# Optimization experiments

Hardware: AMD Instinct MI355X
Metric: run time of the kernel (lower is better)

The kernel has to match this reference:

```python
import jax, jax.numpy as jnp
import numpy as np

NUM_VISUAL = 16
MAX_PATCH = 1024
DIM = 1280
NUM_HEADS = 16
HEAD_DIM = DIM // NUM_HEADS  # 80


def _make_rope_cache(key):
    # cos/sin cache per (visual, patch): (N, P, 1, head_dim*2) = [cos | sin]
    inv_freq = 1.0 / (10000.0 ** (jnp.arange(0, HEAD_DIM, 2, dtype=jnp.float32) / HEAD_DIM))  # (hd/2,)
    pos = jnp.arange(MAX_PATCH, dtype=jnp.float32)  # (P,)
    freqs = pos[:, None] * inv_freq[None, :]              # (P, hd/2)
    emb = jnp.concatenate([freqs, freqs], axis=-1)        # (P, hd)
    cos = jnp.cos(emb)
    sin = jnp.sin(emb)
    cache = jnp.concatenate([cos, sin], axis=-1)          # (P, 2*hd)
    return jnp.broadcast_to(cache[None, :, None, :], (NUM_VISUAL, MAX_PATCH, 1, 2 * HEAD_DIM))


def setup_inputs() -> dict:
    key = jax.random.key(0)
    k1, k2, k3, k4, k5, k6 = jax.random.split(key, 6)
    s = 0.02
    hidden_states = jax.random.normal(k1, (NUM_VISUAL, MAX_PATCH, DIM), dtype=jnp.float32)
    rope_cache = _make_rope_cache(k2)
    seq_lens = jax.random.randint(k3, (NUM_VISUAL,), 512, MAX_PATCH + 1, dtype=jnp.int32)
    w_qkv = jax.random.normal(k4, (3 * DIM, DIM), dtype=jnp.float32) * s
    b_qkv = jnp.zeros((3 * DIM,), dtype=jnp.float32)
    w_proj = jax.random.normal(k5, (DIM, DIM), dtype=jnp.float32) * s
    b_proj = jnp.zeros((DIM,), dtype=jnp.float32)
    return {"hidden_states": hidden_states, "rope_cache": rope_cache, "seq_lens": seq_lens,
            "w_qkv": w_qkv, "b_qkv": b_qkv, "w_proj": w_proj, "b_proj": b_proj}


def _rotate_half(x):
    x1, x2 = jnp.split(x, 2, axis=-1)
    return jnp.concatenate([-x2, x1], axis=-1)


def reference(hidden_states, rope_cache, seq_lens, w_qkv, b_qkv, w_proj, b_proj):
    N, P, D = hidden_states.shape
    H, hd = NUM_HEADS, HEAD_DIM
    # QKV projection: (N, P, 3D) -> (N, P, 3, H, hd)
    qkv = (hidden_states @ w_qkv.T + b_qkv).reshape(N, P, 3, H, hd)
    q, k, v = qkv[:, :, 0], qkv[:, :, 1], qkv[:, :, 2]  # each (N, P, H, hd)
    # RoPE via precomputed cos/sin: rope_cache (N, P, 1, 2*hd)
    cos = rope_cache[..., :hd]   # (N, P, 1, hd), broadcasts over heads
    sin = rope_cache[..., hd:]
    q = q * cos + _rotate_half(q) * sin
    k = k * cos + _rotate_half(k) * sin
    # Attention with key-padding mask (BlockMask equivalent for varlen patches)
    scale = 1.0 / jnp.sqrt(jnp.asarray(hd, dtype=q.dtype))
    scores = jnp.einsum("nqhd,nkhd->nhqk", q, k) * scale  # (N, H, P, P)
    key_valid = jnp.arange(P, dtype=jnp.int32)[None, :] < seq_lens[:, None]  # (N, P)
    neg = jnp.asarray(-1e30, dtype=scores.dtype)
    scores = jnp.where(key_valid[:, None, None, :], scores, neg)
    attn = jax.nn.softmax(scores, axis=-1)
    out = jnp.einsum("nhqk,nkhd->nqhd", attn, v).reshape(N, P, D)
    return out @ w_proj.T + b_proj
```

## Files before the change

kernel.cpp:

```cpp
#include <hip/hip_runtime.h>
#include <stdint.h>

#define DIM     1280
#define NHEADS  16
#define HD      80
#define NV      16
#define MAXP    1024
#define MTOT    (NV*MAXP)

typedef __bf16 bf16;
using bf16x8 = __attribute__((ext_vector_type(8))) __bf16;
using bf16x4 = __attribute__((ext_vector_type(4))) __bf16;
using f32x4  = __attribute__((ext_vector_type(4))) float;

#define GLOAD_LDS16(g, l)                                                     \
    __builtin_amdgcn_global_load_lds(                                         \
        (const __attribute__((address_space(1))) void*)(g),                   \
        (__attribute__((address_space(3))) void*)(l), 16, 0, 0)

__global__ __launch_bounds__(256)
void cvt_bf16(const float* __restrict__ src, bf16* __restrict__ dst, int n4)
{
    const int i = blockIdx.x * 256 + threadIdx.x;
    if (i < n4) {
        const float4 f = ((const float4*)src)[i];
        bf16x4 r;
        r[0] = (bf16)f.x; r[1] = (bf16)f.y; r[2] = (bf16)f.z; r[3] = (bf16)f.w;
        ((bf16x4*)dst)[i] = r;
    }
}

#define GEMM_STAGE(dA, dB, koff) do {                                         \
    GLOAD_LDS16(ga[0] + (koff), (dA) + (0*4 + wave)*512);                     \
    GLOAD_LDS16(gb[0] + (koff), (dB) + (0*4 + wave)*512);                     \
    GLOAD_LDS16(ga[1] + (koff), (dA) + (1*4 + wave)*512);                     \
    GLOAD_LDS16(gb[1] + (koff), (dB) + (1*4 + wave)*512);                     \
    GLOAD_LDS16(ga[2] + (koff), (dA) + (2*4 + wave)*512);                     \
    GLOAD_LDS16(gb[2] + (koff), (dB) + (2*4 + wave)*512);                     \
    GLOAD_LDS16(ga[3] + (koff), (dA) + (3*4 + wave)*512);                     \
    GLOAD_LDS16(gb[3] + (koff), (dB) + (3*4 + wave)*512);                     \
} while (0)

template<bool IS_QKV, int NB, int G>
__global__ __launch_bounds__(256)
void gemm_nt_big(const bf16* __restrict__ A, const bf16* __restrict__ B,
                 const float* __restrict__ bias,
                 bf16* __restrict__ out0, bf16* __restrict__ out1,
                 bf16* __restrict__ out2, float* __restrict__ outf)
{
    const int K = DIM;
    const int NKT = K/64;
    __shared__ __align__(16) bf16 SH[4*128*64];
    bf16* const As0 = SH;
    bf16* const Bs0 = SH + 8192;
    bf16* const As1 = SH + 16384;
    bf16* const Bs1 = SH + 24576;

    const int tid  = threadIdx.x;
    const int lane = tid & 63, wave = tid >> 6;
    const int quad = lane >> 4, c16 = lane & 15;
    const int wm = wave & 1, wn = wave >> 1;

    const int bid = blockIdx.x;
    const int xcd = bid & 7;
    const int idx = bid >> 3;
    const int nbg = idx / (16*G);
    const int rem = idx % (16*G);
    const int mb  = xcd*16 + rem / G;
    const int nb  = nbg*G  + rem % G;

    const int sr   = lane >> 3;
    const int slot = lane & 7;
    const int sc   = (slot ^ sr) * 8;
    const long a_row0 = (long)mb * 128;
    const long b_row0 = (long)nb * 128;

    const bf16* ga[4];
    const bf16* gb[4];
    #pragma unroll
    for (int c = 0; c < 4; ++c) {
        const int seg = c*4 + wave;
        const int row = seg*8 + sr;
        ga[c] = A + (a_row0 + row)*K + sc;
        gb[c] = B + (b_row0 + row)*K + sc;
    }

    f32x4 acc[4][4] = {};
    const int xr = c16 & 7;

    GEMM_STAGE(As0, Bs0, 0);

    for (int kt = 0; kt < NKT; ++kt) {
        const bool odd = kt & 1;
        bf16* const Ac = odd ? As1 : As0;
        bf16* const Bc = odd ? Bs1 : Bs0;
        if (kt + 1 < NKT) {
            bf16* const An = odd ? As0 : As1;
            bf16* const Bn = odd ? Bs0 : Bs1;
            GEMM_STAGE(An, Bn, (kt+1)*64);
            asm volatile("s_waitcnt vmcnt(8)" ::: "memory");
        } else {
            asm volatile("s_waitcnt vmcnt(0)" ::: "memory");
        }
        __builtin_amdgcn_sched_barrier(0);
        __builtin_amdgcn_s_barrier();
        __builtin_amdgcn_sched_barrier(0);

        #pragma unroll
        for (int kk = 0; kk < 2; ++kk) {
            const int j  = kk*4 + quad;
            const int ko = ((j ^ xr) * 8);
            bf16x8 af[4], bfr[4];
            #pragma unroll
            for (int mt = 0; mt < 4; ++mt)
                af[mt] = *(const bf16x8*)(Ac + (wm*64 + mt*16 + c16)*64 + ko);
            #pragma unroll
            for (int nt = 0; nt < 4; ++nt)
                bfr[nt] = *(const bf16x8*)(Bc + (wn*64 + nt*16 + c16)*64 + ko);
            #pragma unroll
            for (int mt = 0; mt < 4; ++mt)
                #pragma unroll
                for (int nt = 0; nt < 4; ++nt)
                    acc[mt][nt] = __builtin_amdgcn_mfma_f32_16x16x32_bf16(
                        af[mt], bfr[nt], acc[mt][nt], 0, 0, 0);
        }

        __builtin_amdgcn_sched_barrier(0);
        __builtin_amdgcn_s_barrier();
        __builtin_amdgcn_sched_barrier(0);
    }

    if constexpr (IS_QKV) {
        const int which = nb / 10;
        if (which < 2) {
            #pragma unroll
            for (int nt = 0; nt < 4; ++nt) {
                const int col = wn*64 + nt*16 + c16;
                const float bv = bias[nb*128 + col];
                #pragma unroll
                for (int mt = 0; mt < 4; ++mt) {
                    #pragma unroll
                    for (int r = 0; r < 4; ++r) {
                        const int row = wm*64 + mt*16 + quad*4 + r;
                        SH[row*128 + (col ^ ((row & 7) << 3))] =
                            (bf16)(acc[mt][nt][r] + bv);
                    }
                }
            }
            __syncthreads();
            bf16* const dst = (which == 0) ? out0 : out1;
            const int n_ = mb >> 3;
            const int pb = (mb & 7) * 128;
            const int j  = tid & 15;
            const int colg = nb*128 - which*DIM + j*8;
            const int hh = colg / 80;
            const int dd = colg - hh*80;
            #pragma unroll
            for (int i = 0; i < 8; ++i) {
                const int p = (tid >> 4) + 16*i;
                bf16x8 v = *(const bf16x8*)(SH + p*128 + ((j ^ (p & 7)) * 8));
                *(bf16x8*)(dst + ((long)((n_*NHEADS + hh)*MAXP + pb + p))*HD + dd) = v;
            }
        } else {
            #pragma unroll
            for (int nt = 0; nt < 4; ++nt) {
                const int dl0 = wn*64 + nt*16 + c16;
                const float bv = bias[nb*128 + dl0];
                const int swz = (dl0 & 15) << 3;
                #pragma unroll
                for (int mt = 0; mt < 4; ++mt) {
                    #pragma unroll
                    for (int r = 0; r < 4; ++r) {
                        const int pl = wm*64 + mt*16 + quad*4 + r;
                        SH[dl0*128 + (pl ^ swz)] = (bf16)(acc[mt][nt][r] + bv);
                    }
                }
            }
            __syncthreads();
            const int n_    = mb >> 3;
            const int pbase = (mb & 7) * 128;
            #pragma unroll
            for (int it = 0; it < 8; ++it) {
                const int c  = tid + 256*it;
                const int dl = c >> 4, j = c & 15;
                const int p0 = (j ^ (dl & 15)) << 3;
                const int rr = (nb - 20)*128 + dl;
                const int hh = rr / HD;
                const int dd = rr - hh*HD;
                bf16x8 v = *(const bf16x8*)(SH + dl*128 + j*8);
                *(bf16x8*)(out2 + ((long)((n_*NHEADS + hh)*HD + dd))*MAXP
                                  + pbase + p0) = v;
            }
        }
    } else {
        #pragma unroll
        for (int nt = 0; nt < 4; ++nt) {
            const int col = nb*128 + wn*64 + nt*16 + c16;
            const float bv = bias[col];
            #pragma unroll
            for (int mt = 0; mt < 4; ++mt) {
                #pragma unroll
                for (int r = 0; r < 4; ++r) {
                    const int row = mb*128 + wm*64 + mt*16 + quad*4 + r;
                    outf[(long)row*DIM + col] = acc[mt][nt][r] + bv;
                }
            }
        }
    }
}

__global__ __launch_bounds__(320)
void rope_kernel(bf16* __restrict__ qb, bf16* __restrict__ kb,
                 const float* __restrict__ rope)
{
    const int tid = threadIdx.x;
    const int j   = tid % 5;
    const int rl  = tid / 5;
    const long grow = (long)blockIdx.x * 64 + rl;
    const int p = (int)(grow & 1023);
    const int h = (int)((grow >> 10) & 15);
    const int n = (int)((grow >> 14) & 15);
    const int a = (int)(grow >> 18);
    bf16* const arr = a ? kb : qb;
    const long base = ((long)((n*NHEADS + h)*MAXP + p))*HD;
    const float* rc = rope + ((long)(n*MAXP + p))*160;
    const int d = j*8;

    bf16x8 x1v = *(const bf16x8*)(arr + base + d);
    bf16x8 x2v = *(const bf16x8*)(arr + base + 40 + d);

    float c1[8], s1[8], c2[8], s2[8];
    *(float4*)(c1)   = *(const float4*)(rc + d);
    *(float4*)(c1+4) = *(const float4*)(rc + d + 4);
    *(float4*)(s1)   = *(const float4*)(rc + 80 + d);
    *(float4*)(s1+4) = *(const float4*)(rc + 80 + d + 4);
    *(float4*)(c2)   = *(const float4*)(rc + 40 + d);
    *(float4*)(c2+4) = *(const float4*)(rc + 40 + d + 4);
    *(float4*)(s2)   = *(const float4*)(rc + 120 + d);
    *(float4*)(s2+4) = *(const float4*)(rc + 120 + d + 4);

    const float QS = 0.11180339887498949f * 1.4426950408889634f;
    bf16x8 r1, r2;
    #pragma unroll
    for (int i = 0; i < 8; ++i) {
        const float x1 = (float)x1v[i];
        const float x2 = (float)x2v[i];
        float o1 = x1 * c1[i] - x2 * s1[i];
        float o2 = x2 * c2[i] + x1 * s2[i];
        if (a == 0) { o1 *= QS; o2 *= QS; }
        r1[i] = (bf16)o1;
        r2[i] = (bf16)o2;
    }
    *(bf16x8*)(arr + base + d)      = r1;
    *(bf16x8*)(arr + base + 40 + d) = r2;
}

#define ATTN_ISSUE(ktp) do {                                                  \
    const long kro_ = qkbase + (long)(ktp)*64*HD;                             \
    kA = k0v ? *(const float4*)(kb + kro_ + (long)kr0*HD + kc0) : zero4;      \
    kB = k1v ? *(const float4*)(kb + kro_ + (long)kr1*HD + kc1) : zero4;      \
    kC = k2v ? *(const float4*)(kb + kro_ + (long)kr2*HD + kc2) : zero4;      \
    const long vro_ = vbase + (long)(ktp)*64 + vc8;                           \
    vA = *(const float4*)(vt + vro_ + (long)vd0*MAXP);                        \
    vB = *(const float4*)(vt + vro_ + (long)vd1*MAXP);                        \
    if (v2ok) vC = *(const float4*)(vt + vro_ + (long)vd2*MAXP);              \
} while (0)

#define ATTN_COMMIT() do {                                                    \
    *(float4*)(Ks + kr0*104 + kc0) = kA;                                      \
    *(float4*)(Ks + kr1*104 + kc1) = kB;                                      \
    *(float4*)(Ks + kr2*104 + kc2) = kC;                                      \
    *(float2*)(Vts + vd0*68 + vc8)     = make_float2(vA.x, vA.y);             \
    *(float2*)(Vts + vd0*68 + vc8 + 4) = make_float2(vA.z, vA.w);             \
    *(float2*)(Vts + vd1*68 + vc8)     = make_float2(vB.x, vB.y);             \
    *(float2*)(Vts + vd1*68 + vc8 + 4) = make_float2(vB.z, vB.w);             \
    if (v2ok) {                                                               \
        *(float2*)(Vts + vd2*68 + vc8)     = make_float2(vC.x, vC.y);         \
        *(float2*)(Vts + vd2*68 + vc8 + 4) = make_float2(vC.z, vC.w);         \
    }                                                                         \
} while (0)

__global__ __launch_bounds__(256)
void attn_kernel(const bf16* __restrict__ qb, const bf16* __restrict__ kb,
                 const bf16* __restrict__ vt, const int* __restrict__ seq_lens,
                 bf16* __restrict__ outb)
{
    __shared__ __align__(16) bf16 Ks[64*104];
    __shared__ __align__(16) bf16 Vts[80*68];

    const int tid  = threadIdx.x;
    const int lane = tid & 63, wave = tid >> 6;
    const int quad = lane >> 4, c16 = lane & 15;
    const int qt = blockIdx.x, h = blockIdx.y, n = blockIdx.z;
    const int seqlen = seq_lens[n];

    const long qkbase = ((long)(n*NHEADS + h)) * MAXP * HD;
    const long vbase  = ((long)(n*NHEADS + h)) * HD * MAXP;

    const float4 zero4 = make_float4(0.f, 0.f, 0.f, 0.f);

    const int kr0 = tid / 12,         kc0 = (tid % 12) * 8;
    const int kr1 = (tid + 256) / 12, kc1 = ((tid + 256) % 12) * 8;
    const int kr2 = (tid + 512) / 12, kc2 = ((tid + 512) % 12) * 8;
    const bool k0v = kc0 < 80, k1v = kc1 < 80, k2v = kc2 < 80;
    const int vd0 = tid >> 3, vd1 = vd0 + 32, vd2 = vd0 + 64;
    const int vc8 = (tid & 7) * 8;
    const bool v2ok = tid < 128;

    float4 kA, kB, kC, vA, vB, vC;

    ATTN_ISSUE(0);
    bf16x8 aq[3];
    {
        const bf16* qrow = qb + qkbase + (long)(qt*64 + wave*16 + c16)*HD + quad*8;
        aq[0] = *(const bf16x8*)(qrow);
        aq[1] = *(const bf16x8*)(qrow + 32);
        aq[2] = *(const bf16x8*)(qrow + 64);
    }

    float mrow = -1e30f, lrow = 0.0f;
    f32x4 O[5] = {};

    union U8 { bf16x8 v; bf16x4 h[2]; };

    const int nkt = (seqlen + 63) >> 6;
    for (int kt = 0; kt < nkt; ++kt) {
        __syncthreads();
        ATTN_COMMIT();
        __syncthreads();
        if (kt + 1 < nkt) ATTN_ISSUE(kt + 1);

        f32x4 S[4] = {};
        __builtin_amdgcn_s_setprio(1);
        #pragma unroll
        for (int kc = 0; kc < 3; ++kc) {
            const int ko = kc*32 + quad*8;
            #pragma unroll
            for (int nt = 0; nt < 4; ++nt) {
                bf16x8 ak = *(const bf16x8*)(Ks + (nt*16 + c16)*104 + ko);
                S[nt] = __builtin_amdgcn_mfma_f32_16x16x32_bf16(ak, aq[kc], S[nt], 0,0,0);
            }
        }
        __builtin_amdgcn_s_setprio(0);

        if (kt == nkt - 1) {
            #pragma unroll
            for (int nt = 0; nt < 4; ++nt) {
                const int key0 = kt*64 + nt*16 + quad*4;
                #pragma unroll
                for (int r = 0; r < 4; ++r)
                    if (key0 + r >= seqlen) S[nt][r] = -1e30f;
            }
        }

        float mx[4];
        #pragma unroll
        for (int nt = 0; nt < 4; ++nt)
            mx[nt] = fmaxf(fmaxf(S[nt][0], S[nt][1]), fmaxf(S[nt][2], S[nt][3]));
        float pmax = fmaxf(fmaxf(mx[0], mx[1]), fmaxf(mx[2], mx[3]));
        pmax = fmaxf(pmax, __shfl_xor(pmax, 16));
        pmax = fmaxf(pmax, __shfl_xor(pmax, 32));

        if (!__all(pmax <= mrow + 8.0f)) {
            const float nm    = fmaxf(mrow, pmax);
            const float alpha = exp2f(mrow - nm);
            mrow = nm;
            lrow *= alpha;
            #pragma unroll
            for (int dt = 0; dt < 5; ++dt)
                #pragma unroll
                for (int r = 0; r < 4; ++r)
                    O[dt][r] *= alpha;
        }

        #pragma unroll
        for (int nt = 0; nt < 4; ++nt)
            #pragma unroll
            for (int r = 0; r < 4; ++r)
                S[nt][r] = exp2f(S[nt][r] - mrow);

        float sm[4];
        #pragma unroll
        for (int nt = 0; nt < 4; ++nt)
            sm[nt] = (S[nt][0] + S[nt][1]) + (S[nt][2] + S[nt][3]);
        float rs = (sm[0] + sm[1]) + (sm[2] + sm[3]);
        rs += __shfl_xor(rs, 16);
        rs += __shfl_xor(rs, 32);
        lrow += rs;

        bf16x8 Pk[2];
        #pragma unroll
        for (int nt = 0; nt < 4; ++nt)
            #pragma unroll
            for (int r = 0; r < 4; ++r)
                Pk[nt >> 1][(nt & 1)*4 + r] = (bf16)S[nt][r];

        __builtin_amdgcn_s_setprio(1);
        #pragma unroll
        for (int kc = 0; kc < 2; ++kc) {
            #pragma unroll
            for (int dt = 0; dt < 5; ++dt) {
                U8 av;
                av.h[0] = *(const bf16x4*)(Vts + (dt*16 + c16)*68 + kc*32 + quad*4);
                av.h[1] = *(const bf16x4*)(Vts + (dt*16 + c16)*68 + kc*32 + 16 + quad*4);
                O[dt] = __builtin_amdgcn_mfma_f32_16x16x32_bf16(av.v, Pk[kc], O[dt], 0,0,0);
            }
        }
        __builtin_amdgcn_s_setprio(0);
    }

    __syncthreads();
    const float inv = 1.0f / lrow;
    #pragma unroll
    for (int dt = 0; dt < 5; ++dt)
        #pragma unroll
        for (int r = 0; r < 4; ++r)
            Ks[(wave*16 + c16)*104 + dt*16 + quad*4 + r] = (bf16)(O[dt][r] * inv);
    __syncthreads();
    for (int i = tid; i < 640; i += 256) {
        const int row = i / 10, c = i % 10;
        const float4 v = *(const float4*)(Ks + row*104 + c*8);
        *(float4*)(outb + ((long)(n*MAXP + qt*64 + row))*DIM + h*HD + c*8) = v;
    }
}

extern "C" void kernel_launch(void* const* d_in, const int* in_sizes, int n_in,
                              void* d_out, int out_size, void* d_ws, size_t ws_size,
                              hipStream_t stream)
{
    const float* hidden = (const float*)d_in[0];
    const float* rope   = (const float*)d_in[1];
    const int*   seql   = (const int*)d_in[2];
    const float* wqkv   = (const float*)d_in[3];
    const float* bqkv   = (const float*)d_in[4];
    const float* wproj  = (const float*)d_in[5];
    const float* bproj  = (const float*)d_in[6];
    float* out = (float*)d_out;

    const size_t H_ELEMS  = (size_t)MTOT*DIM;
    const size_t WQ_ELEMS = (size_t)3*DIM*DIM;
    const size_t WP_ELEMS = (size_t)DIM*DIM;
    const size_t QK_ELEMS = (size_t)NV*NHEADS*MAXP*HD;

    bf16* h_bf  = (bf16*)d_ws;
    bf16* wq_bf = h_bf  + H_ELEMS;
    bf16* wp_bf = wq_bf + WQ_ELEMS;

    bf16* q_b = (bf16*)d_out;
    bf16* k_b = q_b + QK_ELEMS;
    bf16* v_t = (bf16*)d_in[0];
    bf16* a_b = v_t + QK_ELEMS;

    cvt_bf16<<<(H_ELEMS/4 + 255)/256, 256, 0, stream>>>(hidden, h_bf, H_ELEMS/4);
    cvt_bf16<<<(WQ_ELEMS/4 + 255)/256, 256, 0, stream>>>(wqkv, wq_bf, WQ_ELEMS/4);
    cvt_bf16<<<(WP_ELEMS/4 + 255)/256, 256, 0, stream>>>(wproj, wp_bf, WP_ELEMS/4);

    gemm_nt_big<true, 30, 6><<<3840, 256, 0, stream>>>(
        h_bf, wq_bf, bqkv, q_b, k_b, v_t, nullptr);

    rope_kernel<<<524288/64, 320, 0, stream>>>(q_b, k_b, rope);

    attn_kernel<<<dim3(MAXP/64, NHEADS, NV), 256, 0, stream>>>(
        q_b, k_b, v_t, seql, a_b);

    gemm_nt_big<false, 10, 10><<<1280, 256, 0, stream>>>(
        a_b, wp_bf, bproj, nullptr, nullptr, nullptr, out);
}
```

Before: 593.6 us.

## Double attention query tile per block and compute row sums via ones-column MFMA

```diff
diff --git a/kernel.cpp b/kernel.cpp
--- a/kernel.cpp
+++ b/kernel.cpp
@@ -258,35 +258,31 @@
 #define ATTN_ISSUE(ktp) do {                                                  \
     const long kro_ = qkbase + (long)(ktp)*64*HD;                             \
     kA = k0v ? *(const float4*)(kb + kro_ + (long)kr0*HD + kc0) : zero4;      \
-    kB = k1v ? *(const float4*)(kb + kro_ + (long)kr1*HD + kc1) : zero4;      \
-    kC = k2v ? *(const float4*)(kb + kro_ + (long)kr2*HD + kc2) : zero4;      \
+    if (k1on) kB = k1v ? *(const float4*)(kb + kro_ + (long)kr1*HD + kc1) : zero4; \
     const long vro_ = vbase + (long)(ktp)*64 + vc8;                           \
     vA = *(const float4*)(vt + vro_ + (long)vd0*MAXP);                        \
-    vB = *(const float4*)(vt + vro_ + (long)vd1*MAXP);                        \
-    if (v2ok) vC = *(const float4*)(vt + vro_ + (long)vd2*MAXP);              \
+    if (v1on) vB = *(const float4*)(vt + vro_ + (long)vd1*MAXP);              \
 } while (0)
 
 #define ATTN_COMMIT() do {                                                    \
     *(float4*)(Ks + kr0*104 + kc0) = kA;                                      \
-    *(float4*)(Ks + kr1*104 + kc1) = kB;                                      \
-    *(float4*)(Ks + kr2*104 + kc2) = kC;                                      \
+    if (k1on) *(float4*)(Ks + kr1*104 + kc1) = kB;                            \
     *(float2*)(Vts + vd0*68 + vc8)     = make_float2(vA.x, vA.y);             \
     *(float2*)(Vts + vd0*68 + vc8 + 4) = make_float2(vA.z, vA.w);             \
-    *(float2*)(Vts + vd1*68 + vc8)     = make_float2(vB.x, vB.y);             \
-    *(float2*)(Vts + vd1*68 + vc8 + 4) = make_float2(vB.z, vB.w);             \
-    if (v2ok) {                                                               \
-        *(float2*)(Vts + vd2*68 + vc8)     = make_float2(vC.x, vC.y);         \
-        *(float2*)(Vts + vd2*68 + vc8 + 4) = make_float2(vC.z, vC.w);         \
+    if (v1on) {                                                               \
+        *(float2*)(Vts + vd1*68 + vc8)     = make_float2(vB.x, vB.y);         \
+        *(float2*)(Vts + vd1*68 + vc8 + 4) = make_float2(vB.z, vB.w);         \
     }                                                                         \
 } while (0)
 
-__global__ __launch_bounds__(256)
+__global__ __launch_bounds__(512)
 void attn_kernel(const bf16* __restrict__ qb, const bf16* __restrict__ kb,
                  const bf16* __restrict__ vt, const int* __restrict__ seq_lens,
                  bf16* __restrict__ outb)
 {
-    __shared__ __align__(16) bf16 Ks[64*104];
-    __shared__ __align__(16) bf16 Vts[80*68];
+    __shared__ __align__(16) bf16 SM[64*104 + 96*68];
+    bf16* const Ks  = SM;
+    bf16* const Vts = SM + 64*104;
 
     const int tid  = threadIdx.x;
     const int lane = tid & 63, wave = tid >> 6;
@@ -300,26 +296,28 @@
     const float4 zero4 = make_float4(0.f, 0.f, 0.f, 0.f);
 
     const int kr0 = tid / 12,         kc0 = (tid % 12) * 8;
-    const int kr1 = (tid + 256) / 12, kc1 = ((tid + 256) % 12) * 8;
-    const int kr2 = (tid + 512) / 12, kc2 = ((tid + 512) % 12) * 8;
-    const bool k0v = kc0 < 80, k1v = kc1 < 80, k2v = kc2 < 80;
-    const int vd0 = tid >> 3, vd1 = vd0 + 32, vd2 = vd0 + 64;
+    const int kr1 = (tid + 512) / 12, kc1 = ((tid + 512) % 12) * 8;
+    const bool k0v = kc0 < 80, k1v = kc1 < 80;
+    const bool k1on = tid < 256;
+    const int vd0 = tid >> 3, vd1 = vd0 + 64;
     const int vc8 = (tid & 7) * 8;
-    const bool v2ok = tid < 128;
-
-    float4 kA, kB, kC, vA, vB, vC;
-
+    const bool v1on = tid < 128;
+
+    float4 kA, kB, vA, vB;
+
+    for (int i = tid; i < 16*68; i += 512)
+        Vts[80*68 + i] = (bf16)1.0f;
     ATTN_ISSUE(0);
     bf16x8 aq[3];
     {
-        const bf16* qrow = qb + qkbase + (long)(qt*64 + wave*16 + c16)*HD + quad*8;
+        const bf16* qrow = qb + qkbase + (long)(qt*128 + wave*16 + c16)*HD + quad*8;
         aq[0] = *(const bf16x8*)(qrow);
         aq[1] = *(const bf16x8*)(qrow + 32);
         aq[2] = *(const bf16x8*)(qrow + 64);
     }
 
-    float mrow = -1e30f, lrow = 0.0f;
-    f32x4 O[5] = {};
+    float mrow = -1e30f;
+    f32x4 O[6] = {};
 
     union U8 { bf16x8 v; bf16x4 h[2]; };
 
@@ -365,9 +363,8 @@
             const float nm    = fmaxf(mrow, pmax);
             const float alpha = exp2f(mrow - nm);
             mrow = nm;
-            lrow *= alpha;
-            #pragma unroll
-            for (int dt = 0; dt < 5; ++dt)
+            #pragma unroll
+            for (int dt = 0; dt < 6; ++dt)
                 #pragma unroll
                 for (int r = 0; r < 4; ++r)
                     O[dt][r] *= alpha;
@@ -379,15 +376,6 @@
             for (int r = 0; r < 4; ++r)
                 S[nt][r] = exp2f(S[nt][r] - mrow);
 
-        float sm[4];
-        #pragma unroll
-        for (int nt = 0; nt < 4; ++nt)
-            sm[nt] = (S[nt][0] + S[nt][1]) + (S[nt][2] + S[nt][3]);
-        float rs = (sm[0] + sm[1]) + (sm[2] + sm[3]);
-        rs += __shfl_xor(rs, 16);
-        rs += __shfl_xor(rs, 32);
-        lrow += rs;
-
         bf16x8 Pk[2];
         #pragma unroll
         for (int nt = 0; nt < 4; ++nt)
@@ -399,7 +387,7 @@
         #pragma unroll
         for (int kc = 0; kc < 2; ++kc) {
             #pragma unroll
-            for (int dt = 0; dt < 5; ++dt) {
+            for (int dt = 0; dt < 6; ++dt) {
                 U8 av;
                 av.h[0] = *(const bf16x4*)(Vts + (dt*16 + c16)*68 + kc*32 + quad*4);
                 av.h[1] = *(const bf16x4*)(Vts + (dt*16 + c16)*68 + kc*32 + 16 + quad*4);
@@ -410,17 +398,17 @@
     }
 
     __syncthreads();
-    const float inv = 1.0f / lrow;
+    const float inv = 1.0f / O[5][0];
     #pragma unroll
     for (int dt = 0; dt < 5; ++dt)
         #pragma unroll
         for (int r = 0; r < 4; ++r)
-            Ks[(wave*16 + c16)*104 + dt*16 + quad*4 + r] = (bf16)(O[dt][r] * inv);
+            SM[(wave*16 + c16)*88 + dt*16 + quad*4 + r] = (bf16)(O[dt][r] * inv);
     __syncthreads();
-    for (int i = tid; i < 640; i += 256) {
+    for (int i = tid; i < 1280; i += 512) {
         const int row = i / 10, c = i % 10;
-        const float4 v = *(const float4*)(Ks + row*104 + c*8);
-        *(float4*)(outb + ((long)(n*MAXP + qt*64 + row))*DIM + h*HD + c*8) = v;
+        const float4 v = *(const float4*)(SM + row*88 + c*8);
+        *(float4*)(outb + ((long)(n*MAXP + qt*128 + row))*DIM + h*HD + c*8) = v;
     }
 }
 
@@ -460,7 +448,7 @@
 
     rope_kernel<<<524288/64, 320, 0, stream>>>(q_b, k_b, rope);
 
-    attn_kernel<<<dim3(MAXP/64, NHEADS, NV), 256, 0, stream>>>(
+    attn_kernel<<<dim3(MAXP/128, NHEADS, NV), 512, 0, stream>>>(
         q_b, k_b, v_t, seql, a_b);
 
     gemm_nt_big<false, 10, 10><<<1280, 256, 0, stream>>>(
```

New measurement: 556.7 us. 6.2% less time.
